# Performance work log

Measured on AMD Instinct MI355X. Metric: run time of the kernel, lower is better.

## Reference

```python
import jax, jax.numpy as jnp
import numpy as np

B, N, D_IN, D, E, MAXD = 16, 512, 256, 64, 32, 50
LN_EPS = 1e-5

def setup_inputs() -> dict:
    key = jax.random.key(0)
    ks = jax.random.split(key, 24)
    s = lambda fan: 1.0 / np.sqrt(fan)
    inp = {
        'x': jax.random.normal(ks[0], (B, N, D_IN), jnp.float32),
        'price_rising_ranks': jax.random.randint(ks[1], (B, N), 0, N, jnp.int64),
        'Wp': jax.random.normal(ks[2], (D_IN, D), jnp.float32) * s(D_IN),
        'bp': jnp.zeros((D,), jnp.float32),
        'Wq': jax.random.normal(ks[3], (D, D), jnp.float32) * s(D),
        'bq': jnp.zeros((D,), jnp.float32),
        'Wk': jax.random.normal(ks[4], (D, D), jnp.float32) * s(D),
        'bk': jnp.zeros((D,), jnp.float32),
        'Wv': jax.random.normal(ks[5], (D, D), jnp.float32) * s(D),
        'bv': jnp.zeros((D,), jnp.float32),
        'Eemb': jax.random.normal(ks[6], (MAXD + 1, E), jnp.float32),
        'Wr1': jax.random.normal(ks[7], (E, 16), jnp.float32) * s(E),
        'br1': jnp.zeros((16,), jnp.float32),
        'Wr2': jax.random.normal(ks[8], (16, 1), jnp.float32) * s(16),
        'Wf1': jax.random.normal(ks[9], (D, 2 * D), jnp.float32) * s(D),
        'bf1': jnp.zeros((2 * D,), jnp.float32),
        'Wf2': jax.random.normal(ks[10], (2 * D, D), jnp.float32) * s(2 * D),
        'bf2': jnp.zeros((D,), jnp.float32),
        'ln_g': jnp.ones((D,), jnp.float32),
        'ln_b': jnp.zeros((D,), jnp.float32),
        'Ws1': jax.random.normal(ks[11], (D, 32), jnp.float32) * s(D),
        'bs1': jnp.zeros((32,), jnp.float32),
        'Ws2': jax.random.normal(ks[12], (32, 1), jnp.float32) * s(32),
        'bs2': jnp.zeros((1,), jnp.float32),
    }
    return inp

def reference(x, price_rising_ranks, Wp, bp, Wq, bq, Wk, bk, Wv, bv,
              Eemb, Wr1, br1, Wr2, Wf1, bf1, Wf2, bf2, ln_g, ln_b,
              Ws1, bs1, Ws2, bs2):
    xp = x @ Wp + bp                                  # (B,N,D)
    q = xp @ Wq + bq
    k = xp @ Wk + bk
    v = xp @ Wv + bv
    scores = jnp.einsum('bnd,bmd->bnm', q, k) / jnp.sqrt(jnp.float32(D))
    # rank-distance pairwise bias
    r = price_rising_ranks
    dists = jnp.clip(jnp.abs(r[:, :, None] - r[:, None, :]), 0, MAXD)  # (B,N,N) int
    emb = Eemb[dists]                                 # (B,N,N,E)
    w = jax.nn.relu(emb @ Wr1 + br1) @ Wr2            # (B,N,N,1)
    rel = jax.nn.sigmoid(w[..., 0])                   # (B,N,N)
    scores = scores * rel
    attn = jax.nn.softmax(scores, axis=-1)
    ao = jnp.einsum('bnm,bmd->bnd', attn, v)
    # feed forward + layernorm
    h = jax.nn.relu(ao @ Wf1 + bf1) @ Wf2 + bf2
    mu = jnp.mean(h, axis=-1, keepdims=True)
    var = jnp.mean((h - mu) ** 2, axis=-1, keepdims=True)
    hn = (h - mu) / jnp.sqrt(var + LN_EPS) * ln_g + ln_b
    # score projection
    out = jax.nn.relu(hn @ Ws1 + bs1) @ Ws2 + bs2     # (B,N,1)
    return jax.nn.sigmoid(out[..., 0])                # (B,N)
```

## Files before the change

### kernel.cpp

```cpp
#include <hip/hip_runtime.h>

using f32x4 = __attribute__((ext_vector_type(4))) float;
using s16x8 = __attribute__((ext_vector_type(8))) short;

static __device__ __forceinline__ unsigned short f2bf(float f){
  union { float f; unsigned int i; } c; c.f = f;
  return (unsigned short)((c.i + 0x7FFFu + ((c.i >> 16) & 1u)) >> 16);
}
static __device__ __forceinline__ s16x8 ld8(const unsigned short* p){
  return *(const s16x8*)p;
}
static __device__ __forceinline__ s16x8 cvt8(const float* p){
  const float4* q = (const float4*)p;
  float4 a = q[0], b = q[1];
  s16x8 r;
  r[0]=(short)f2bf(a.x); r[1]=(short)f2bf(a.y); r[2]=(short)f2bf(a.z); r[3]=(short)f2bf(a.w);
  r[4]=(short)f2bf(b.x); r[5]=(short)f2bf(b.y); r[6]=(short)f2bf(b.z); r[7]=(short)f2bf(b.w);
  return r;
}
static __device__ __forceinline__ f32x4 mfma16(s16x8 a, s16x8 b, f32x4 c){
  return __builtin_amdgcn_mfma_f32_16x16x32_bf16(a, b, c, 0, 0, 0);
}

__global__ __launch_bounds__(192) void k_proj(const float* __restrict__ x,
    const float* __restrict__ Wp, const float* __restrict__ bp,
    const float* __restrict__ Wq, const float* __restrict__ bq,
    const float* __restrict__ Wk, const float* __restrict__ bk,
    const float* __restrict__ Wv, const float* __restrict__ bv,
    const float* __restrict__ Ee, const float* __restrict__ Wr1,
    const float* __restrict__ br1, const float* __restrict__ Wr2,
    unsigned short* __restrict__ q, unsigned short* __restrict__ kk,
    unsigned short* __restrict__ vt, float* __restrict__ rel_t)
{
  __shared__ __align__(16) unsigned short WpT[64*264];
  __shared__ __align__(16) unsigned short Wt3[3][64*72];
  __shared__ __align__(16) unsigned short xs[2][16*72];

  int t = threadIdx.x;
  int row0b = blockIdx.x*32;

  const float4* xb4 = (const float4*)(x + row0b*256);
  float4 tc0 = xb4[((t*2  ) & 255)*8];
  float4 tc1 = xb4[((t*2+1) & 255)*8];

  const float4* Wp4 = (const float4*)Wp;
  for (int i = t; i < 4096; i += 192){
    float4 v = Wp4[i];
    int k = i >> 4, n = (i & 15) * 4;
    WpT[(n+0)*264+k] = f2bf(v.x);
    WpT[(n+1)*264+k] = f2bf(v.y);
    WpT[(n+2)*264+k] = f2bf(v.z);
    WpT[(n+3)*264+k] = f2bf(v.w);
  }
  const float4* Wq4 = (const float4*)Wq;
  const float4* Wk4 = (const float4*)Wk;
  const float4* Wv4 = (const float4*)Wv;
  for (int i = t; i < 1024; i += 192){
    int k = i >> 4, n = (i & 15) * 4;
    float4 a = Wq4[i], b2 = Wk4[i], c2 = Wv4[i];
    Wt3[0][(n+0)*72+k]=f2bf(a.x);  Wt3[0][(n+1)*72+k]=f2bf(a.y);
    Wt3[0][(n+2)*72+k]=f2bf(a.z);  Wt3[0][(n+3)*72+k]=f2bf(a.w);
    Wt3[1][(n+0)*72+k]=f2bf(b2.x); Wt3[1][(n+1)*72+k]=f2bf(b2.y);
    Wt3[1][(n+2)*72+k]=f2bf(b2.z); Wt3[1][(n+3)*72+k]=f2bf(b2.w);
    Wt3[2][(n+0)*72+k]=f2bf(c2.x); Wt3[2][(n+1)*72+k]=f2bf(c2.y);
    Wt3[2][(n+2)*72+k]=f2bf(c2.z); Wt3[2][(n+3)*72+k]=f2bf(c2.w);
  }
  if (blockIdx.x == 0 && t >= 128 && t < 179){
    int dd = t - 128;
    float e[32];
    const float4* e4 = (const float4*)(Ee + dd*32);
#pragma unroll
    for (int j = 0; j < 8; ++j){
      float4 v = e4[j];
      e[j*4+0]=v.x; e[j*4+1]=v.y; e[j*4+2]=v.z; e[j*4+3]=v.w;
    }
    float w = 0.f;
    for (int h = 0; h < 16; ++h){
      float s = br1[h];
#pragma unroll
      for (int j = 0; j < 32; ++j) s += e[j] * Wr1[j*16 + h];
      w += fmaxf(s, 0.f) * Wr2[h];
    }
    rel_t[dd] = 1.f / (1.f + __expf(-w));
  }
  asm volatile("" :: "v"(tc0.x), "v"(tc1.x));
  __syncthreads();

  if (t < 128){
    int lane = t & 63, wave = t >> 6, colL = lane & 15, quad = lane >> 4;
    int row0 = row0b + wave*16;

    const float* xr = x + (row0 + colL)*256;
    f32x4 acc[4] = {};
    for (int kc = 0; kc < 256; kc += 32){
      s16x8 a = cvt8(xr + kc + quad*8);
#pragma unroll
      for (int nt = 0; nt < 4; ++nt)
        acc[nt] = mfma16(a, ld8(&WpT[(nt*16+colL)*264 + kc + quad*8]), acc[nt]);
    }
    unsigned short* xw = xs[wave];
#pragma unroll
    for (int nt = 0; nt < 4; ++nt){
      int col = nt*16 + colL;
      float bb = bp[col];
#pragma unroll
      for (int i = 0; i < 4; ++i)
        xw[(quad*4+i)*72 + col] = f2bf(acc[nt][i] + bb);
    }
    s16x8 a0 = ld8(&xw[colL*72 +  0 + quad*8]);
    s16x8 a1 = ld8(&xw[colL*72 + 32 + quad*8]);

#pragma unroll
    for (int w = 0; w < 3; ++w){
      const float* bias = w==0 ? bq : (w==1 ? bk : bv);
      f32x4 c[4] = {};
#pragma unroll
      for (int nt = 0; nt < 4; ++nt){
        c[nt] = mfma16(a0, ld8(&Wt3[w][(nt*16+colL)*72 +  0 + quad*8]), c[nt]);
        c[nt] = mfma16(a1, ld8(&Wt3[w][(nt*16+colL)*72 + 32 + quad*8]), c[nt]);
      }
#pragma unroll
      for (int nt = 0; nt < 4; ++nt){
        int col = nt*16 + colL;
        float bb = bias[col];
#pragma unroll
        for (int i = 0; i < 4; ++i){
          int row = row0 + quad*4 + i;
          float v = c[nt][i] + bb;
          if (w == 0)      q [row*64 + col] = f2bf(v);
          else if (w == 1) kk[row*64 + col] = f2bf(v);
          else             vt[(row>>9)*32768 + col*512 + (row & 511)] = f2bf(v);
        }
      }
    }
  }
}

__global__ __launch_bounds__(256) void k_attn_ffn(const unsigned short* __restrict__ q,
    const unsigned short* __restrict__ kmat, const unsigned short* __restrict__ vt,
    const int* __restrict__ ranks, const float* __restrict__ rel_t,
    const float* __restrict__ Wf1, const float* __restrict__ bf1,
    const float* __restrict__ Wf2, const float* __restrict__ bf2,
    const float* __restrict__ lng, const float* __restrict__ lnb,
    const float* __restrict__ Ws1, const float* __restrict__ bs1,
    const float* __restrict__ Ws2, const float* __restrict__ bs2,
    float* __restrict__ out)
{
  __shared__ __align__(16) int r_s[512];
  __shared__ float rt_s[64];
  __shared__ float pmax_s[4][16], psum_s[4][16];
  __shared__ __align__(16) unsigned short Pbuf[4*16*136];
  __shared__ __align__(16) float Opart[4][16*66];
  __shared__ __align__(16) unsigned short Wf1t[128*72];
  __shared__ __align__(16) unsigned short Wf2t[64*136];
  __shared__ __align__(16) unsigned short Ws1t[32*72];
  __shared__ float cb[384];

  int b = blockIdx.y, qt = blockIdx.x;
  int t = threadIdx.x, lane = t & 63, wave = t >> 6;
  int colL = lane & 15, quad = lane >> 4;

  if (t < 128) ((int4*)r_s)[t] = ((const int4*)(ranks + b*512))[t];
  if (t < 64) rt_s[t] = (t < 51) ? rel_t[t] : 0.f;
  const float4* Wf14 = (const float4*)Wf1;
  for (int i = t; i < 2048; i += 256){
    float4 v = Wf14[i];
    int d = i >> 5, j = (i & 31) * 4;
    Wf1t[(j+0)*72+d]=f2bf(v.x); Wf1t[(j+1)*72+d]=f2bf(v.y);
    Wf1t[(j+2)*72+d]=f2bf(v.z); Wf1t[(j+3)*72+d]=f2bf(v.w);
  }
  const float4* Wf24 = (const float4*)Wf2;
  for (int i = t; i < 2048; i += 256){
    float4 v = Wf24[i];
    int kx = i >> 4, n = (i & 15) * 4;
    Wf2t[(n+0)*136+kx]=f2bf(v.x); Wf2t[(n+1)*136+kx]=f2bf(v.y);
    Wf2t[(n+2)*136+kx]=f2bf(v.z); Wf2t[(n+3)*136+kx]=f2bf(v.w);
  }
  const float4* Ws14 = (const float4*)Ws1;
  for (int i = t; i < 512; i += 256){
    float4 v = Ws14[i];
    int d = i >> 3, c0 = (i & 7) * 4;
    Ws1t[(c0+0)*72+d]=f2bf(v.x); Ws1t[(c0+1)*72+d]=f2bf(v.y);
    Ws1t[(c0+2)*72+d]=f2bf(v.z); Ws1t[(c0+3)*72+d]=f2bf(v.w);
  }
  if (t < 128) cb[t] = bf1[t];
  if (t < 64){ cb[128+t] = bf2[t]; cb[192+t] = lng[t]; cb[256+t] = lnb[t]; }
  if (t < 32){ cb[320+t] = bs1[t]; cb[352+t] = Ws2[t]; }

  int qrow0 = qt*16;
  const unsigned short* qp = q    + b*32768;
  const unsigned short* kp = kmat + b*32768;
  const unsigned short* vp = vt   + b*32768;

  s16x8 aq0 = ld8(qp + (qrow0+colL)*64 +  0 + quad*8);
  s16x8 aq1 = ld8(qp + (qrow0+colL)*64 + 32 + quad*8);

  int key0 = wave*128;
  f32x4 S[8];
#pragma unroll
  for (int mt = 0; mt < 8; ++mt){
    int key = key0 + mt*16 + colL;
    f32x4 c = {};
    c = mfma16(aq0, ld8(kp + key*64 +  0 + quad*8), c);
    c = mfma16(aq1, ld8(kp + key*64 + 32 + quad*8), c);
    S[mt] = c;
  }
  __syncthreads();

  int rq[4];
#pragma unroll
  for (int i = 0; i < 4; ++i) rq[i] = r_s[qrow0 + quad*4 + i];

  float rmax[4] = {-1e30f,-1e30f,-1e30f,-1e30f};
#pragma unroll
  for (int mt = 0; mt < 8; ++mt){
    int rm = r_s[key0 + mt*16 + colL];
#pragma unroll
    for (int i = 0; i < 4; ++i){
      int dd = rq[i] - rm; dd = dd < 0 ? -dd : dd; dd = dd > 50 ? 50 : dd;
      float s = S[mt][i] * 0.125f * rt_s[dd];
      S[mt][i] = s;
      rmax[i] = fmaxf(rmax[i], s);
    }
  }
#pragma unroll
  for (int i = 0; i < 4; ++i){
    rmax[i] = fmaxf(rmax[i], __shfl_xor(rmax[i], 1));
    rmax[i] = fmaxf(rmax[i], __shfl_xor(rmax[i], 2));
    rmax[i] = fmaxf(rmax[i], __shfl_xor(rmax[i], 4));
    rmax[i] = fmaxf(rmax[i], __shfl_xor(rmax[i], 8));
  }
  if (colL == 0){
#pragma unroll
    for (int i = 0; i < 4; ++i) pmax_s[wave][quad*4 + i] = rmax[i];
  }
  __syncthreads();
  float gmax[4];
#pragma unroll
  for (int i = 0; i < 4; ++i){
    int r = quad*4 + i;
    gmax[i] = fmaxf(fmaxf(pmax_s[0][r], pmax_s[1][r]), fmaxf(pmax_s[2][r], pmax_s[3][r]));
  }
  float rsum[4] = {0.f,0.f,0.f,0.f};
#pragma unroll
  for (int mt = 0; mt < 8; ++mt){
#pragma unroll
    for (int i = 0; i < 4; ++i){
      float p = __expf(S[mt][i] - gmax[i]);
      S[mt][i] = p;
      rsum[i] += p;
    }
  }
#pragma unroll
  for (int i = 0; i < 4; ++i){
    rsum[i] += __shfl_xor(rsum[i], 1);
    rsum[i] += __shfl_xor(rsum[i], 2);
    rsum[i] += __shfl_xor(rsum[i], 4);
    rsum[i] += __shfl_xor(rsum[i], 8);
  }
  if (colL == 0){
#pragma unroll
    for (int i = 0; i < 4; ++i) psum_s[wave][quad*4 + i] = rsum[i];
  }
  __syncthreads();
  float inv[4];
#pragma unroll
  for (int i = 0; i < 4; ++i){
    int r = quad*4 + i;
    inv[i] = 1.f / (psum_s[0][r] + psum_s[1][r] + psum_s[2][r] + psum_s[3][r]);
  }
  unsigned short* Pw = Pbuf + wave*(16*136);
#pragma unroll
  for (int mt = 0; mt < 8; ++mt){
#pragma unroll
    for (int i = 0; i < 4; ++i)
      Pw[(quad*4+i)*136 + mt*16 + colL] = f2bf(S[mt][i] * inv[i]);
  }
  f32x4 O[4] = {};
#pragma unroll
  for (int mc = 0; mc < 128; mc += 32){
    s16x8 ap = ld8(&Pw[colL*136 + mc + quad*8]);
#pragma unroll
    for (int dt = 0; dt < 4; ++dt)
      O[dt] = mfma16(ap, ld8(vp + (dt*16+colL)*512 + key0 + mc + quad*8), O[dt]);
  }
  float* Ow = Opart[wave];
#pragma unroll
  for (int dt = 0; dt < 4; ++dt)
#pragma unroll
    for (int i = 0; i < 4; ++i)
      Ow[(quad*4+i)*66 + dt*16 + colL] = O[dt][i];
  __syncthreads();
  unsigned short* aoS = Pbuf;
  for (int e = t; e < 1024; e += 256){
    int row = e >> 6, col = e & 63;
    float s = Opart[0][row*66+col] + Opart[1][row*66+col]
            + Opart[2][row*66+col] + Opart[3][row*66+col];
    aoS[row*72 + col] = f2bf(s);
  }
  __syncthreads();

  if (wave == 0){
    unsigned short* hw = Pbuf + 2176;
    int row0g = b*512 + qt*16;

    f32x4 a1[8] = {};
#pragma unroll
    for (int kc = 0; kc < 64; kc += 32){
      s16x8 a = ld8(&aoS[colL*72 + kc + quad*8]);
#pragma unroll
      for (int nt = 0; nt < 8; ++nt)
        a1[nt] = mfma16(a, ld8(&Wf1t[(nt*16+colL)*72 + kc + quad*8]), a1[nt]);
    }
#pragma unroll
    for (int nt = 0; nt < 8; ++nt){
      int col = nt*16 + colL;
      float bb = cb[col];
#pragma unroll
      for (int i = 0; i < 4; ++i)
        hw[(quad*4+i)*136 + col] = f2bf(fmaxf(a1[nt][i] + bb, 0.f));
    }
    f32x4 a2[4] = {};
#pragma unroll
    for (int kc = 0; kc < 128; kc += 32){
      s16x8 a = ld8(&hw[colL*136 + kc + quad*8]);
#pragma unroll
      for (int nt = 0; nt < 4; ++nt)
        a2[nt] = mfma16(a, ld8(&Wf2t[(nt*16+colL)*136 + kc + quad*8]), a2[nt]);
    }
    float vals[4][4];
#pragma unroll
    for (int nt = 0; nt < 4; ++nt){
      float bb = cb[128 + nt*16 + colL];
#pragma unroll
      for (int i = 0; i < 4; ++i) vals[i][nt] = a2[nt][i] + bb;
    }
    float hnv[4][4];
#pragma unroll
    for (int i = 0; i < 4; ++i){
      float s = vals[i][0]+vals[i][1]+vals[i][2]+vals[i][3];
      s += __shfl_xor(s,1); s += __shfl_xor(s,2); s += __shfl_xor(s,4); s += __shfl_xor(s,8);
      float mu = s * (1.f/64.f);
      float d0=vals[i][0]-mu, d1=vals[i][1]-mu, d2=vals[i][2]-mu, d3=vals[i][3]-mu;
      float s2 = d0*d0 + d1*d1 + d2*d2 + d3*d3;
      s2 += __shfl_xor(s2,1); s2 += __shfl_xor(s2,2); s2 += __shfl_xor(s2,4); s2 += __shfl_xor(s2,8);
      float invs = rsqrtf(s2*(1.f/64.f) + 1e-5f);
#pragma unroll
      for (int nt = 0; nt < 4; ++nt){
        int col = nt*16 + colL;
        hnv[i][nt] = (vals[i][nt]-mu)*invs*cb[192+col] + cb[256+col];
      }
    }
#pragma unroll
    for (int i = 0; i < 4; ++i)
#pragma unroll
      for (int nt = 0; nt < 4; ++nt)
        hw[(quad*4+i)*72 + nt*16 + colL] = f2bf(hnv[i][nt]);

    f32x4 a3[2] = {};
#pragma unroll
    for (int kc = 0; kc < 64; kc += 32){
      s16x8 a = ld8(&hw[colL*72 + kc + quad*8]);
#pragma unroll
      for (int nt = 0; nt < 2; ++nt)
        a3[nt] = mfma16(a, ld8(&Ws1t[(nt*16+colL)*72 + kc + quad*8]), a3[nt]);
    }
    float bs2f = bs2[0];
#pragma unroll
    for (int i = 0; i < 4; ++i){
      float p = 0.f;
#pragma unroll
      for (int nt = 0; nt < 2; ++nt){
        int col = nt*16 + colL;
        p += fmaxf(a3[nt][i] + cb[320+col], 0.f) * cb[352+col];
      }
      p += __shfl_xor(p,1); p += __shfl_xor(p,2); p += __shfl_xor(p,4); p += __shfl_xor(p,8);
      if (colL == 0){
        float z = p + bs2f;
        out[row0g + quad*4 + i] = 1.f / (1.f + __expf(-z));
      }
    }
  }
}

extern "C" void kernel_launch(void* const* d_in, const int* in_sizes, int n_in,
                              void* d_out, int out_size, void* d_ws, size_t ws_size,
                              hipStream_t stream)
{
  const float* x    = (const float*)d_in[0];
  const int*   rank = (const int*)d_in[1];
  const float* Wp   = (const float*)d_in[2];
  const float* bp   = (const float*)d_in[3];
  const float* Wq   = (const float*)d_in[4];
  const float* bq   = (const float*)d_in[5];
  const float* Wk   = (const float*)d_in[6];
  const float* bk   = (const float*)d_in[7];
  const float* Wv   = (const float*)d_in[8];
  const float* bv   = (const float*)d_in[9];
  const float* Ee   = (const float*)d_in[10];
  const float* Wr1  = (const float*)d_in[11];
  const float* br1  = (const float*)d_in[12];
  const float* Wr2  = (const float*)d_in[13];
  const float* Wf1  = (const float*)d_in[14];
  const float* bf1  = (const float*)d_in[15];
  const float* Wf2  = (const float*)d_in[16];
  const float* bf2  = (const float*)d_in[17];
  const float* lng  = (const float*)d_in[18];
  const float* lnb  = (const float*)d_in[19];
  const float* Ws1  = (const float*)d_in[20];
  const float* bs1  = (const float*)d_in[21];
  const float* Ws2  = (const float*)d_in[22];
  const float* bs2  = (const float*)d_in[23];
  float* out = (float*)d_out;

  char* ws = (char*)d_ws;
  float*          rel_t = (float*)(ws + 0);
  unsigned short* q     = (unsigned short*)(ws + 256);
  unsigned short* kk    = (unsigned short*)(ws + 256 + 1*1048576);
  unsigned short* vt    = (unsigned short*)(ws + 256 + 2*1048576);

  k_proj<<<dim3(256), dim3(192), 0, stream>>>(x, Wp, bp, Wq, bq, Wk, bk, Wv, bv,
                                              Ee, Wr1, br1, Wr2, q, kk, vt, rel_t);
  k_attn_ffn<<<dim3(32, 16), dim3(256), 0, stream>>>(q, kk, vt, rank, rel_t,
                                              Wf1, bf1, Wf2, bf2, lng, lnb,
                                              Ws1, bs1, Ws2, bs2, out);
}
```

Measured before the change: 136.1 us.

## Hoist weight bf16 conversion into a prep kernel, read transposed weights from global

Adds a k_prep kernel that converts and transposes all weight matrices to bf16 once, and packs the biases, into the workspace. k_proj and k_attn_ffn then read the pre-transposed weights directly from global memory (through cache) instead of every block redoing the fp32-to-bf16 transpose into LDS. This removes redundant per-block conversion work and LDS use, which may raise occupancy. In exchange it adds a kernel launch, and the MFMA B-operand loads become global/L2 reads rather than LDS reads.

```diff
diff --git a/kernel.cpp b/kernel.cpp
--- a/kernel.cpp
+++ b/kernel.cpp
@@ -22,128 +22,133 @@
   return __builtin_amdgcn_mfma_f32_16x16x32_bf16(a, b, c, 0, 0, 0);
 }
 
-__global__ __launch_bounds__(192) void k_proj(const float* __restrict__ x,
-    const float* __restrict__ Wp, const float* __restrict__ bp,
-    const float* __restrict__ Wq, const float* __restrict__ bq,
-    const float* __restrict__ Wk, const float* __restrict__ bk,
-    const float* __restrict__ Wv, const float* __restrict__ bv,
+__global__ __launch_bounds__(256) void k_prep(
+    const float* __restrict__ Wp, const float* __restrict__ Wq,
+    const float* __restrict__ Wk, const float* __restrict__ Wv,
     const float* __restrict__ Ee, const float* __restrict__ Wr1,
     const float* __restrict__ br1, const float* __restrict__ Wr2,
-    unsigned short* __restrict__ q, unsigned short* __restrict__ kk,
-    unsigned short* __restrict__ vt, float* __restrict__ rel_t)
-{
-  __shared__ __align__(16) unsigned short WpT[64*264];
-  __shared__ __align__(16) unsigned short Wt3[3][64*72];
-  __shared__ __align__(16) unsigned short xs[2][16*72];
-
-  int t = threadIdx.x;
-  int row0b = blockIdx.x*32;
-
-  const float4* xb4 = (const float4*)(x + row0b*256);
-  float4 tc0 = xb4[((t*2  ) & 255)*8];
-  float4 tc1 = xb4[((t*2+1) & 255)*8];
-
-  const float4* Wp4 = (const float4*)Wp;
-  for (int i = t; i < 4096; i += 192){
-    float4 v = Wp4[i];
-    int k = i >> 4, n = (i & 15) * 4;
-    WpT[(n+0)*264+k] = f2bf(v.x);
-    WpT[(n+1)*264+k] = f2bf(v.y);
-    WpT[(n+2)*264+k] = f2bf(v.z);
-    WpT[(n+3)*264+k] = f2bf(v.w);
-  }
-  const float4* Wq4 = (const float4*)Wq;
-  const float4* Wk4 = (const float4*)Wk;
-  const float4* Wv4 = (const float4*)Wv;
-  for (int i = t; i < 1024; i += 192){
-    int k = i >> 4, n = (i & 15) * 4;
-    float4 a = Wq4[i], b2 = Wk4[i], c2 = Wv4[i];
-    Wt3[0][(n+0)*72+k]=f2bf(a.x);  Wt3[0][(n+1)*72+k]=f2bf(a.y);
-    Wt3[0][(n+2)*72+k]=f2bf(a.z);  Wt3[0][(n+3)*72+k]=f2bf(a.w);
-    Wt3[1][(n+0)*72+k]=f2bf(b2.x); Wt3[1][(n+1)*72+k]=f2bf(b2.y);
-    Wt3[1][(n+2)*72+k]=f2bf(b2.z); Wt3[1][(n+3)*72+k]=f2bf(b2.w);
-    Wt3[2][(n+0)*72+k]=f2bf(c2.x); Wt3[2][(n+1)*72+k]=f2bf(c2.y);
-    Wt3[2][(n+2)*72+k]=f2bf(c2.z); Wt3[2][(n+3)*72+k]=f2bf(c2.w);
-  }
-  if (blockIdx.x == 0 && t >= 128 && t < 179){
-    int dd = t - 128;
-    float e[32];
-    const float4* e4 = (const float4*)(Ee + dd*32);
-#pragma unroll
-    for (int j = 0; j < 8; ++j){
-      float4 v = e4[j];
-      e[j*4+0]=v.x; e[j*4+1]=v.y; e[j*4+2]=v.z; e[j*4+3]=v.w;
-    }
-    float w = 0.f;
-    for (int h = 0; h < 16; ++h){
-      float s = br1[h];
-#pragma unroll
-      for (int j = 0; j < 32; ++j) s += e[j] * Wr1[j*16 + h];
-      w += fmaxf(s, 0.f) * Wr2[h];
-    }
-    rel_t[dd] = 1.f / (1.f + __expf(-w));
-  }
-  asm volatile("" :: "v"(tc0.x), "v"(tc1.x));
-  __syncthreads();
-
-  if (t < 128){
-    int lane = t & 63, wave = t >> 6, colL = lane & 15, quad = lane >> 4;
-    int row0 = row0b + wave*16;
-
-    const float* xr = x + (row0 + colL)*256;
-    f32x4 acc[4] = {};
-    for (int kc = 0; kc < 256; kc += 32){
-      s16x8 a = cvt8(xr + kc + quad*8);
-#pragma unroll
-      for (int nt = 0; nt < 4; ++nt)
-        acc[nt] = mfma16(a, ld8(&WpT[(nt*16+colL)*264 + kc + quad*8]), acc[nt]);
-    }
-    unsigned short* xw = xs[wave];
-#pragma unroll
-    for (int nt = 0; nt < 4; ++nt){
-      int col = nt*16 + colL;
-      float bb = bp[col];
-#pragma unroll
-      for (int i = 0; i < 4; ++i)
-        xw[(quad*4+i)*72 + col] = f2bf(acc[nt][i] + bb);
-    }
-    s16x8 a0 = ld8(&xw[colL*72 +  0 + quad*8]);
-    s16x8 a1 = ld8(&xw[colL*72 + 32 + quad*8]);
-
-#pragma unroll
-    for (int w = 0; w < 3; ++w){
-      const float* bias = w==0 ? bq : (w==1 ? bk : bv);
-      f32x4 c[4] = {};
-#pragma unroll
-      for (int nt = 0; nt < 4; ++nt){
-        c[nt] = mfma16(a0, ld8(&Wt3[w][(nt*16+colL)*72 +  0 + quad*8]), c[nt]);
-        c[nt] = mfma16(a1, ld8(&Wt3[w][(nt*16+colL)*72 + 32 + quad*8]), c[nt]);
-      }
-#pragma unroll
-      for (int nt = 0; nt < 4; ++nt){
-        int col = nt*16 + colL;
-        float bb = bias[col];
-#pragma unroll
-        for (int i = 0; i < 4; ++i){
-          int row = row0 + quad*4 + i;
-          float v = c[nt][i] + bb;
-          if (w == 0)      q [row*64 + col] = f2bf(v);
-          else if (w == 1) kk[row*64 + col] = f2bf(v);
-          else             vt[(row>>9)*32768 + col*512 + (row & 511)] = f2bf(v);
-        }
-      }
-    }
-  }
-}
-
-__global__ __launch_bounds__(256) void k_attn_ffn(const unsigned short* __restrict__ q,
-    const unsigned short* __restrict__ kmat, const unsigned short* __restrict__ vt,
-    const int* __restrict__ ranks, const float* __restrict__ rel_t,
     const float* __restrict__ Wf1, const float* __restrict__ bf1,
     const float* __restrict__ Wf2, const float* __restrict__ bf2,
     const float* __restrict__ lng, const float* __restrict__ lnb,
     const float* __restrict__ Ws1, const float* __restrict__ bs1,
     const float* __restrict__ Ws2, const float* __restrict__ bs2,
+    unsigned short* __restrict__ wpt, unsigned short* __restrict__ wqt,
+    unsigned short* __restrict__ wkt, unsigned short* __restrict__ wvt,
+    unsigned short* __restrict__ wf1t, unsigned short* __restrict__ wf2t,
+    unsigned short* __restrict__ ws1t, float* __restrict__ cbp,
+    float* __restrict__ rel_t)
+{
+  int g = blockIdx.x*256 + threadIdx.x;
+  { int e = g; wpt[(e&63)*256 + (e>>6)] = f2bf(Wp[e]); }
+  if (g < 4096){
+    int e = g, n = e & 63, k = e >> 6;
+    wqt[n*64 + k] = f2bf(Wq[e]);
+    wkt[n*64 + k] = f2bf(Wk[e]);
+    wvt[n*64 + k] = f2bf(Wv[e]);
+  }
+  if (g < 8192){
+    int e = g;
+    wf1t[(e&127)*64 + (e>>7)] = f2bf(Wf1[e]);
+    wf2t[(e&63)*128 + (e>>6)] = f2bf(Wf2[e]);
+  }
+  if (g < 2048) ws1t[(g&31)*64 + (g>>5)] = f2bf(Ws1[g]);
+  if (g >= 8192 && g < 8577){
+    int u = g - 8192; float v;
+    if      (u < 128) v = bf1[u];
+    else if (u < 192) v = bf2[u-128];
+    else if (u < 256) v = lng[u-192];
+    else if (u < 320) v = lnb[u-256];
+    else if (u < 352) v = bs1[u-320];
+    else if (u < 384) v = Ws2[u-352];
+    else              v = bs2[0];
+    cbp[u] = v;
+  }
+  if (g >= 8704 && g < 8755){
+    int dd = g - 8704;
+    float e[32];
+    const float4* e4 = (const float4*)(Ee + dd*32);
+#pragma unroll
+    for (int j = 0; j < 8; ++j){
+      float4 v = e4[j];
+      e[j*4+0]=v.x; e[j*4+1]=v.y; e[j*4+2]=v.z; e[j*4+3]=v.w;
+    }
+    float w = 0.f;
+    for (int h = 0; h < 16; ++h){
+      float s = br1[h];
+#pragma unroll
+      for (int j = 0; j < 32; ++j) s += e[j] * Wr1[j*16 + h];
+      w += fmaxf(s, 0.f) * Wr2[h];
+    }
+    rel_t[dd] = 1.f / (1.f + __expf(-w));
+  }
+}
+
+__global__ __launch_bounds__(128) void k_proj(const float* __restrict__ x,
+    const float* __restrict__ bp, const float* __restrict__ bq,
+    const float* __restrict__ bk, const float* __restrict__ bv,
+    const unsigned short* __restrict__ wpt, const unsigned short* __restrict__ wqt,
+    const unsigned short* __restrict__ wkt, const unsigned short* __restrict__ wvt,
+    unsigned short* __restrict__ q, unsigned short* __restrict__ kk,
+    unsigned short* __restrict__ vt)
+{
+  __shared__ __align__(16) unsigned short xs[2][16*72];
+
+  int t = threadIdx.x, lane = t & 63, wave = t >> 6;
+  int colL = lane & 15, quad = lane >> 4;
+  int row0 = blockIdx.x*32 + wave*16;
+
+  const float* xr = x + (row0 + colL)*256;
+  f32x4 acc[4] = {};
+#pragma unroll
+  for (int kc = 0; kc < 256; kc += 32){
+    s16x8 a = cvt8(xr + kc + quad*8);
+#pragma unroll
+    for (int nt = 0; nt < 4; ++nt)
+      acc[nt] = mfma16(a, ld8(&wpt[(nt*16+colL)*256 + kc + quad*8]), acc[nt]);
+  }
+  unsigned short* xw = xs[wave];
+#pragma unroll
+  for (int nt = 0; nt < 4; ++nt){
+    int col = nt*16 + colL;
+    float bb = bp[col];
+#pragma unroll
+    for (int i = 0; i < 4; ++i)
+      xw[(quad*4+i)*72 + col] = f2bf(acc[nt][i] + bb);
+  }
+  s16x8 a0 = ld8(&xw[colL*72 +  0 + quad*8]);
+  s16x8 a1 = ld8(&xw[colL*72 + 32 + quad*8]);
+
+#pragma unroll
+  for (int w = 0; w < 3; ++w){
+    const float* bias = w==0 ? bq : (w==1 ? bk : bv);
+    const unsigned short* Wt = w==0 ? wqt : (w==1 ? wkt : wvt);
+    f32x4 c[4] = {};
+#pragma unroll
+    for (int nt = 0; nt < 4; ++nt){
+      c[nt] = mfma16(a0, ld8(&Wt[(nt*16+colL)*64 +  0 + quad*8]), c[nt]);
+      c[nt] = mfma16(a1, ld8(&Wt[(nt*16+colL)*64 + 32 + quad*8]), c[nt]);
+    }
+#pragma unroll
+    for (int nt = 0; nt < 4; ++nt){
+      int col = nt*16 + colL;
+      float bb = bias[col];
+#pragma unroll
+      for (int i = 0; i < 4; ++i){
+        int row = row0 + quad*4 + i;
+        float v = c[nt][i] + bb;
+        if (w == 0)      q [row*64 + col] = f2bf(v);
+        else if (w == 1) kk[row*64 + col] = f2bf(v);
+        else             vt[(row>>9)*32768 + col*512 + (row & 511)] = f2bf(v);
+      }
+    }
+  }
+}
+
+__global__ __launch_bounds__(256) void k_attn_ffn(const unsigned short* __restrict__ q,
+    const unsigned short* __restrict__ kmat, const unsigned short* __restrict__ vt,
+    const int* __restrict__ ranks, const float* __restrict__ rel_t,
+    const unsigned short* __restrict__ wf1t, const unsigned short* __restrict__ wf2t,
+    const unsigned short* __restrict__ ws1t, const float* __restrict__ cbp,
     float* __restrict__ out)
 {
   __shared__ __align__(16) int r_s[512];
@@ -151,10 +156,7 @@
   __shared__ float pmax_s[4][16], psum_s[4][16];
   __shared__ __align__(16) unsigned short Pbuf[4*16*136];
   __shared__ __align__(16) float Opart[4][16*66];
-  __shared__ __align__(16) unsigned short Wf1t[128*72];
-  __shared__ __align__(16) unsigned short Wf2t[64*136];
-  __shared__ __align__(16) unsigned short Ws1t[32*72];
-  __shared__ float cb[384];
+  __shared__ float cb[388];
 
   int b = blockIdx.y, qt = blockIdx.x;
   int t = threadIdx.x, lane = t & 63, wave = t >> 6;
@@ -162,30 +164,11 @@
 
   if (t < 128) ((int4*)r_s)[t] = ((const int4*)(ranks + b*512))[t];
   if (t < 64) rt_s[t] = (t < 51) ? rel_t[t] : 0.f;
-  const float4* Wf14 = (const float4*)Wf1;
-  for (int i = t; i < 2048; i += 256){
-    float4 v = Wf14[i];
-    int d = i >> 5, j = (i & 31) * 4;
-    Wf1t[(j+0)*72+d]=f2bf(v.x); Wf1t[(j+1)*72+d]=f2bf(v.y);
-    Wf1t[(j+2)*72+d]=f2bf(v.z); Wf1t[(j+3)*72+d]=f2bf(v.w);
-  }
-  const float4* Wf24 = (const float4*)Wf2;
-  for (int i = t; i < 2048; i += 256){
-    float4 v = Wf24[i];
-    int kx = i >> 4, n = (i & 15) * 4;
-    Wf2t[(n+0)*136+kx]=f2bf(v.x); Wf2t[(n+1)*136+kx]=f2bf(v.y);
-    Wf2t[(n+2)*136+kx]=f2bf(v.z); Wf2t[(n+3)*136+kx]=f2bf(v.w);
-  }
-  const float4* Ws14 = (const float4*)Ws1;
-  for (int i = t; i < 512; i += 256){
-    float4 v = Ws14[i];
-    int d = i >> 3, c0 = (i & 7) * 4;
-    Ws1t[(c0+0)*72+d]=f2bf(v.x); Ws1t[(c0+1)*72+d]=f2bf(v.y);
-    Ws1t[(c0+2)*72+d]=f2bf(v.z); Ws1t[(c0+3)*72+d]=f2bf(v.w);
-  }
-  if (t < 128) cb[t] = bf1[t];
-  if (t < 64){ cb[128+t] = bf2[t]; cb[192+t] = lng[t]; cb[256+t] = lnb[t]; }
-  if (t < 32){ cb[320+t] = bs1[t]; cb[352+t] = Ws2[t]; }
+  if (t >= 64 && t < 161){
+    int u = t - 64;
+    if (u < 96) ((float4*)cb)[u] = ((const float4*)cbp)[u];
+    else        cb[384] = cbp[384];
+  }
 
   int qrow0 = qt*16;
   const unsigned short* qp = q    + b*32768;
@@ -310,7 +293,7 @@
       s16x8 a = ld8(&aoS[colL*72 + kc + quad*8]);
 #pragma unroll
       for (int nt = 0; nt < 8; ++nt)
-        a1[nt] = mfma16(a, ld8(&Wf1t[(nt*16+colL)*72 + kc + quad*8]), a1[nt]);
+        a1[nt] = mfma16(a, ld8(&wf1t[(nt*16+colL)*64 + kc + quad*8]), a1[nt]);
     }
 #pragma unroll
     for (int nt = 0; nt < 8; ++nt){
@@ -326,7 +309,7 @@
       s16x8 a = ld8(&hw[colL*136 + kc + quad*8]);
 #pragma unroll
       for (int nt = 0; nt < 4; ++nt)
-        a2[nt] = mfma16(a, ld8(&Wf2t[(nt*16+colL)*136 + kc + quad*8]), a2[nt]);
+        a2[nt] = mfma16(a, ld8(&wf2t[(nt*16+colL)*128 + kc + quad*8]), a2[nt]);
     }
     float vals[4][4];
 #pragma unroll
@@ -363,9 +346,9 @@
       s16x8 a = ld8(&hw[colL*72 + kc + quad*8]);
 #pragma unroll
       for (int nt = 0; nt < 2; ++nt)
-        a3[nt] = mfma16(a, ld8(&Ws1t[(nt*16+colL)*72 + kc + quad*8]), a3[nt]);
-    }
-    float bs2f = bs2[0];
+        a3[nt] = mfma16(a, ld8(&ws1t[(nt*16+colL)*64 + kc + quad*8]), a3[nt]);
+    }
+    float bs2f = cb[384];
 #pragma unroll
     for (int i = 0; i < 4; ++i){
       float p = 0.f;
@@ -418,10 +401,22 @@
   unsigned short* q     = (unsigned short*)(ws + 256);
   unsigned short* kk    = (unsigned short*)(ws + 256 + 1*1048576);
   unsigned short* vt    = (unsigned short*)(ws + 256 + 2*1048576);
-
-  k_proj<<<dim3(256), dim3(192), 0, stream>>>(x, Wp, bp, Wq, bq, Wk, bk, Wv, bv,
-                                              Ee, Wr1, br1, Wr2, q, kk, vt, rel_t);
+  unsigned short* wpt   = (unsigned short*)(ws + 3145984);
+  unsigned short* wqt   = (unsigned short*)(ws + 3178752);
+  unsigned short* wkt   = (unsigned short*)(ws + 3186944);
+  unsigned short* wvt   = (unsigned short*)(ws + 3195136);
+  unsigned short* wf1t  = (unsigned short*)(ws + 3203328);
+  unsigned short* wf2t  = (unsigned short*)(ws + 3219712);
+  unsigned short* ws1t  = (unsigned short*)(ws + 3236096);
+  float*          cbp   = (float*)(ws + 3240192);
+
+  k_prep<<<dim3(64), dim3(256), 0, stream>>>(Wp, Wq, Wk, Wv, Ee, Wr1, br1, Wr2,
+                                             Wf1, bf1, Wf2, bf2, lng, lnb,
+                                             Ws1, bs1, Ws2, bs2,
+                                             wpt, wqt, wkt, wvt, wf1t, wf2t, ws1t,
+                                             cbp, rel_t);
+  k_proj<<<dim3(256), dim3(128), 0, stream>>>(x, bp, bq, bk, bv,
+                                              wpt, wqt, wkt, wvt, q, kk, vt);
   k_attn_ffn<<<dim3(32, 16), dim3(256), 0, stream>>>(q, kk, vt, rank, rel_t,
-                                              Wf1, bf1, Wf2, bf2, lng, lnb,
-                                              Ws1, bs1, Ws2, bs2, out);
-}
+                                              wf1t, wf2t, ws1t, cbp, out);
+}
```

Result: faster. 131.9 us (-3.0%).

## Pre-convert FFN weights to bf16 once in projection kernel, read from global

Applied to the files above, without the earlier changes.

Moves the fp32-to-bf16 transpose of Wf1, Wf2, Ws1 and the packing of small bias vectors out of each of the 512 attention blocks and into the projection kernel, which has spare threads spread across its 256 blocks. The attention kernel then reads the pre-transposed bf16 weights straight from global/L2 in its MFMA loops instead of staging them in LDS. This cuts redundant per-block weight conversion and LDS use, which may raise occupancy, but the FFN MFMAs now do uncoalesced-ish global loads. It also widens the projection block to 256 threads, changes the cache-touch prefetch, and unrolls the Wp k-loop.

```diff
diff --git a/kernel.cpp b/kernel.cpp
--- a/kernel.cpp
+++ b/kernel.cpp
@@ -22,29 +22,35 @@
   return __builtin_amdgcn_mfma_f32_16x16x32_bf16(a, b, c, 0, 0, 0);
 }
 
-__global__ __launch_bounds__(192) void k_proj(const float* __restrict__ x,
+__global__ __launch_bounds__(256) void k_proj(const float* __restrict__ x,
     const float* __restrict__ Wp, const float* __restrict__ bp,
     const float* __restrict__ Wq, const float* __restrict__ bq,
     const float* __restrict__ Wk, const float* __restrict__ bk,
     const float* __restrict__ Wv, const float* __restrict__ bv,
     const float* __restrict__ Ee, const float* __restrict__ Wr1,
     const float* __restrict__ br1, const float* __restrict__ Wr2,
+    const float* __restrict__ Wf1, const float* __restrict__ bf1,
+    const float* __restrict__ Wf2, const float* __restrict__ bf2,
+    const float* __restrict__ lng, const float* __restrict__ lnb,
+    const float* __restrict__ Ws1, const float* __restrict__ bs1,
+    const float* __restrict__ Ws2, const float* __restrict__ bs2,
     unsigned short* __restrict__ q, unsigned short* __restrict__ kk,
-    unsigned short* __restrict__ vt, float* __restrict__ rel_t)
+    unsigned short* __restrict__ vt,
+    unsigned short* __restrict__ wf1t, unsigned short* __restrict__ wf2t,
+    unsigned short* __restrict__ ws1t, float* __restrict__ cbp,
+    float* __restrict__ rel_t)
 {
   __shared__ __align__(16) unsigned short WpT[64*264];
   __shared__ __align__(16) unsigned short Wt3[3][64*72];
   __shared__ __align__(16) unsigned short xs[2][16*72];
 
-  int t = threadIdx.x;
-  int row0b = blockIdx.x*32;
-
-  const float4* xb4 = (const float4*)(x + row0b*256);
-  float4 tc0 = xb4[((t*2  ) & 255)*8];
-  float4 tc1 = xb4[((t*2+1) & 255)*8];
+  int t = threadIdx.x, bid = blockIdx.x;
+  int row0b = bid*32;
+
+  float tc = x[row0b*256 + t*32];
 
   const float4* Wp4 = (const float4*)Wp;
-  for (int i = t; i < 4096; i += 192){
+  for (int i = t; i < 4096; i += 256){
     float4 v = Wp4[i];
     int k = i >> 4, n = (i & 15) * 4;
     WpT[(n+0)*264+k] = f2bf(v.x);
@@ -55,7 +61,7 @@
   const float4* Wq4 = (const float4*)Wq;
   const float4* Wk4 = (const float4*)Wk;
   const float4* Wv4 = (const float4*)Wv;
-  for (int i = t; i < 1024; i += 192){
+  for (int i = t; i < 1024; i += 256){
     int k = i >> 4, n = (i & 15) * 4;
     float4 a = Wq4[i], b2 = Wk4[i], c2 = Wv4[i];
     Wt3[0][(n+0)*72+k]=f2bf(a.x);  Wt3[0][(n+1)*72+k]=f2bf(a.y);
@@ -65,25 +71,51 @@
     Wt3[2][(n+0)*72+k]=f2bf(c2.x); Wt3[2][(n+1)*72+k]=f2bf(c2.y);
     Wt3[2][(n+2)*72+k]=f2bf(c2.z); Wt3[2][(n+3)*72+k]=f2bf(c2.w);
   }
-  if (blockIdx.x == 0 && t >= 128 && t < 179){
-    int dd = t - 128;
-    float e[32];
-    const float4* e4 = (const float4*)(Ee + dd*32);
-#pragma unroll
-    for (int j = 0; j < 8; ++j){
-      float4 v = e4[j];
-      e[j*4+0]=v.x; e[j*4+1]=v.y; e[j*4+2]=v.z; e[j*4+3]=v.w;
-    }
-    float w = 0.f;
-    for (int h = 0; h < 16; ++h){
-      float s = br1[h];
-#pragma unroll
-      for (int j = 0; j < 32; ++j) s += e[j] * Wr1[j*16 + h];
-      w += fmaxf(s, 0.f) * Wr2[h];
-    }
-    rel_t[dd] = 1.f / (1.f + __expf(-w));
-  }
-  asm volatile("" :: "v"(tc0.x), "v"(tc1.x));
+
+  if (t >= 128){
+    int u = t - 128;
+    if (u < 32){
+      int e = bid*32 + u;
+      wf1t[(e&127)*64 + (e>>7)] = f2bf(Wf1[e]);
+    } else if (u < 64){
+      int e = bid*32 + (u-32);
+      wf2t[(e&63)*128 + (e>>6)] = f2bf(Wf2[e]);
+    } else if (u < 72){
+      int e = bid*8 + (u-64);
+      ws1t[(e&31)*64 + (e>>5)] = f2bf(Ws1[e]);
+    } else if (u < 76){
+      int idx = bid*4 + (u-72);
+      if (idx < 385){
+        float v;
+        if      (idx < 128) v = bf1[idx];
+        else if (idx < 192) v = bf2[idx-128];
+        else if (idx < 256) v = lng[idx-192];
+        else if (idx < 320) v = lnb[idx-256];
+        else if (idx < 352) v = bs1[idx-320];
+        else if (idx < 384) v = Ws2[idx-352];
+        else                v = bs2[0];
+        cbp[idx] = v;
+      }
+    } else if (bid == 1 && u >= 76 && u < 127){
+      int dd = u - 76;
+      float e[32];
+      const float4* e4 = (const float4*)(Ee + dd*32);
+#pragma unroll
+      for (int j = 0; j < 8; ++j){
+        float4 v = e4[j];
+        e[j*4+0]=v.x; e[j*4+1]=v.y; e[j*4+2]=v.z; e[j*4+3]=v.w;
+      }
+      float w = 0.f;
+      for (int h = 0; h < 16; ++h){
+        float s = br1[h];
+#pragma unroll
+        for (int j = 0; j < 32; ++j) s += e[j] * Wr1[j*16 + h];
+        w += fmaxf(s, 0.f) * Wr2[h];
+      }
+      rel_t[dd] = 1.f / (1.f + __expf(-w));
+    }
+  }
+  asm volatile("" :: "v"(tc));
   __syncthreads();
 
   if (t < 128){
@@ -92,6 +124,7 @@
 
     const float* xr = x + (row0 + colL)*256;
     f32x4 acc[4] = {};
+#pragma unroll
     for (int kc = 0; kc < 256; kc += 32){
       s16x8 a = cvt8(xr + kc + quad*8);
 #pragma unroll
@@ -139,11 +172,8 @@
 __global__ __launch_bounds__(256) void k_attn_ffn(const unsigned short* __restrict__ q,
     const unsigned short* __restrict__ kmat, const unsigned short* __restrict__ vt,
     const int* __restrict__ ranks, const float* __restrict__ rel_t,
-    const float* __restrict__ Wf1, const float* __restrict__ bf1,
-    const float* __restrict__ Wf2, const float* __restrict__ bf2,
-    const float* __restrict__ lng, const float* __restrict__ lnb,
-    const float* __restrict__ Ws1, const float* __restrict__ bs1,
-    const float* __restrict__ Ws2, const float* __restrict__ bs2,
+    const unsigned short* __restrict__ wf1t, const unsigned short* __restrict__ wf2t,
+    const unsigned short* __restrict__ ws1t, const float* __restrict__ cbp,
     float* __restrict__ out)
 {
   __shared__ __align__(16) int r_s[512];
@@ -151,10 +181,7 @@
   __shared__ float pmax_s[4][16], psum_s[4][16];
   __shared__ __align__(16) unsigned short Pbuf[4*16*136];
   __shared__ __align__(16) float Opart[4][16*66];
-  __shared__ __align__(16) unsigned short Wf1t[128*72];
-  __shared__ __align__(16) unsigned short Wf2t[64*136];
-  __shared__ __align__(16) unsigned short Ws1t[32*72];
-  __shared__ float cb[384];
+  __shared__ float cb[388];
 
   int b = blockIdx.y, qt = blockIdx.x;
   int t = threadIdx.x, lane = t & 63, wave = t >> 6;
@@ -162,30 +189,11 @@
 
   if (t < 128) ((int4*)r_s)[t] = ((const int4*)(ranks + b*512))[t];
   if (t < 64) rt_s[t] = (t < 51) ? rel_t[t] : 0.f;
-  const float4* Wf14 = (const float4*)Wf1;
-  for (int i = t; i < 2048; i += 256){
-    float4 v = Wf14[i];
-    int d = i >> 5, j = (i & 31) * 4;
-    Wf1t[(j+0)*72+d]=f2bf(v.x); Wf1t[(j+1)*72+d]=f2bf(v.y);
-    Wf1t[(j+2)*72+d]=f2bf(v.z); Wf1t[(j+3)*72+d]=f2bf(v.w);
-  }
-  const float4* Wf24 = (const float4*)Wf2;
-  for (int i = t; i < 2048; i += 256){
-    float4 v = Wf24[i];
-    int kx = i >> 4, n = (i & 15) * 4;
-    Wf2t[(n+0)*136+kx]=f2bf(v.x); Wf2t[(n+1)*136+kx]=f2bf(v.y);
-    Wf2t[(n+2)*136+kx]=f2bf(v.z); Wf2t[(n+3)*136+kx]=f2bf(v.w);
-  }
-  const float4* Ws14 = (const float4*)Ws1;
-  for (int i = t; i < 512; i += 256){
-    float4 v = Ws14[i];
-    int d = i >> 3, c0 = (i & 7) * 4;
-    Ws1t[(c0+0)*72+d]=f2bf(v.x); Ws1t[(c0+1)*72+d]=f2bf(v.y);
-    Ws1t[(c0+2)*72+d]=f2bf(v.z); Ws1t[(c0+3)*72+d]=f2bf(v.w);
-  }
-  if (t < 128) cb[t] = bf1[t];
-  if (t < 64){ cb[128+t] = bf2[t]; cb[192+t] = lng[t]; cb[256+t] = lnb[t]; }
-  if (t < 32){ cb[320+t] = bs1[t]; cb[352+t] = Ws2[t]; }
+  if (t >= 64 && t < 161){
+    int u = t - 64;
+    if (u < 96) ((float4*)cb)[u] = ((const float4*)cbp)[u];
+    else        cb[384] = cbp[384];
+  }
 
   int qrow0 = qt*16;
   const unsigned short* qp = q    + b*32768;
@@ -310,7 +318,7 @@
       s16x8 a = ld8(&aoS[colL*72 + kc + quad*8]);
 #pragma unroll
       for (int nt = 0; nt < 8; ++nt)
-        a1[nt] = mfma16(a, ld8(&Wf1t[(nt*16+colL)*72 + kc + quad*8]), a1[nt]);
+        a1[nt] = mfma16(a, ld8(&wf1t[(nt*16+colL)*64 + kc + quad*8]), a1[nt]);
     }
 #pragma unroll
     for (int nt = 0; nt < 8; ++nt){
@@ -326,7 +334,7 @@
       s16x8 a = ld8(&hw[colL*136 + kc + quad*8]);
 #pragma unroll
       for (int nt = 0; nt < 4; ++nt)
-        a2[nt] = mfma16(a, ld8(&Wf2t[(nt*16+colL)*136 + kc + quad*8]), a2[nt]);
+        a2[nt] = mfma16(a, ld8(&wf2t[(nt*16+colL)*128 + kc + quad*8]), a2[nt]);
     }
     float vals[4][4];
 #pragma unroll
@@ -363,9 +371,9 @@
       s16x8 a = ld8(&hw[colL*72 + kc + quad*8]);
 #pragma unroll
       for (int nt = 0; nt < 2; ++nt)
-        a3[nt] = mfma16(a, ld8(&Ws1t[(nt*16+colL)*72 + kc + quad*8]), a3[nt]);
-    }
-    float bs2f = bs2[0];
+        a3[nt] = mfma16(a, ld8(&ws1t[(nt*16+colL)*64 + kc + quad*8]), a3[nt]);
+    }
+    float bs2f = cb[384];
 #pragma unroll
     for (int i = 0; i < 4; ++i){
       float p = 0.f;
@@ -418,10 +426,17 @@
   unsigned short* q     = (unsigned short*)(ws + 256);
   unsigned short* kk    = (unsigned short*)(ws + 256 + 1*1048576);
   unsigned short* vt    = (unsigned short*)(ws + 256 + 2*1048576);
-
-  k_proj<<<dim3(256), dim3(192), 0, stream>>>(x, Wp, bp, Wq, bq, Wk, bk, Wv, bv,
-                                              Ee, Wr1, br1, Wr2, q, kk, vt, rel_t);
+  unsigned short* wf1t  = (unsigned short*)(ws + 3203328);
+  unsigned short* wf2t  = (unsigned short*)(ws + 3219712);
+  unsigned short* ws1t  = (unsigned short*)(ws + 3236096);
+  float*          cbp   = (float*)(ws + 3240192);
+
+  k_proj<<<dim3(256), dim3(256), 0, stream>>>(x, Wp, bp, Wq, bq, Wk, bk, Wv, bv,
+                                              Ee, Wr1, br1, Wr2,
+                                              Wf1, bf1, Wf2, bf2, lng, lnb,
+                                              Ws1, bs1, Ws2, bs2,
+                                              q, kk, vt,
+                                              wf1t, wf2t, ws1t, cbp, rel_t);
   k_attn_ffn<<<dim3(32, 16), dim3(256), 0, stream>>>(q, kk, vt, rank, rel_t,
-                                              Wf1, bf1, Wf2, bf2, lng, lnb,
-                                              Ws1, bs1, Ws2, bs2, out);
-}
+                                              wf1t, wf2t, ws1t, cbp, out);
+}
```

Result: faster. 132.8 us (-2.4%).
